# Optimization experiments

Measured on AMD Instinct MI355X. Metric: run time of the kernel, lower is better.

## Reference

```python
import jax, jax.numpy as jnp
import numpy as np

M, Q, H, L = 1, 9, 512, 2

def lstm_seq(x, w_ih, w_hh, b, reverse=False):
    # x: [B, T, Din] -> outputs [B, T, H], final (h, c) each [B, H]
    B = x.shape[0]
    h0 = jnp.zeros((B, H), x.dtype)
    xw = jnp.einsum('btd,gd->btg', x, w_ih) + b  # [B, T, 4H] input projection, precomputed
    def step(carry, xt):
        h, c = carry
        g = xt + h @ w_hh.T
        i, f, gg, o = jnp.split(g, 4, axis=-1)  # torch gate order: i, f, g, o
        c = jax.nn.sigmoid(f) * c + jax.nn.sigmoid(i) * jnp.tanh(gg)
        h = jax.nn.sigmoid(o) * jnp.tanh(c)
        return (h, c), h
    (hT, cT), hs = jax.lax.scan(step, (h0, h0), jnp.swapaxes(xw, 0, 1), reverse=reverse)
    return jnp.swapaxes(hs, 0, 1), hT, cT

def _forward(X, future_features, Y_teacher,
             enc_w_ih_l0, enc_w_hh_l0, enc_b_l0, enc_w_ih_l0r, enc_w_hh_l0r, enc_b_l0r,
             enc_w_ih_l1, enc_w_hh_l1, enc_b_l1, enc_w_ih_l1r, enc_w_hh_l1r, enc_b_l1r,
             dec_w_ih_l0, dec_w_hh_l0, dec_b_l0, dec_w_ih_l1, dec_w_hh_l1, dec_b_l1,
             bidi_w_h, bidi_b_h, out_w, out_b, horizon_span):
    B = X.shape[0]
    enc = [((enc_w_ih_l0, enc_w_hh_l0, enc_b_l0), (enc_w_ih_l0r, enc_w_hh_l0r, enc_b_l0r)),
           ((enc_w_ih_l1, enc_w_hh_l1, enc_b_l1), (enc_w_ih_l1r, enc_w_hh_l1r, enc_b_l1r))]
    inp, hs, cs = X, [], []
    for fw, bw in enc:  # bidirectional multilayer encoder
        of, hf, cf = lstm_seq(inp, *fw, reverse=False)
        ob, hb, cb = lstm_seq(inp, *bw, reverse=True)
        inp = jnp.concatenate([of, ob], axis=-1)
        hs += [hf, hb]; cs += [cf, cb]
    h = jnp.stack(hs)  # [2L, B, H], torch order (l0_fwd, l0_bwd, l1_fwd, l1_bwd)
    c = jnp.stack(cs)
    def merge(s):  # NOTE: original applies bidi_project__h / nonlin__h to BOTH h and c
        s = s.reshape(L, 2, B, H)
        s = jnp.concatenate([s[:, 0], s[:, 1]], axis=2)       # [L, B, 2H]
        s = jnp.swapaxes(s, 0, 1).reshape(B, 2 * L * H)
        s = jax.nn.elu(s @ bidi_w_h.T + bidi_b_h)             # [B, L*H]
        return jnp.swapaxes(s.reshape(B, L, H), 0, 1)         # [L, B, H]
    h, c = merge(h), merge(c)
    dec = [(dec_w_ih_l0, dec_w_hh_l0, dec_b_l0), (dec_w_ih_l1, dec_w_hh_l1, dec_b_l1)]
    def dec_step(carry, f_t):
        h, c, y_prev = carry
        x = jnp.concatenate([y_prev, f_t], axis=-1)  # [B, M + d_future_features]
        nh, nc = [], []
        for l, (w_ih, w_hh, b) in enumerate(dec):
            g = x @ w_ih.T + h[l] @ w_hh.T + b
            i, f, gg, o = jnp.split(g, 4, axis=-1)
            cl = jax.nn.sigmoid(f) * c[l] + jax.nn.sigmoid(i) * jnp.tanh(gg)
            x = jax.nn.sigmoid(o) * jnp.tanh(cl)
            nh.append(x); nc.append(cl)
        y = x @ out_w.T + out_b                       # [B, M*Q]
        return (jnp.stack(nh), jnp.stack(nc), y[:, :M]), y
    y0 = X[:, -1, :M]
    _, ys = jax.lax.scan(dec_step, (h, c, y0), jnp.swapaxes(future_features, 0, 1))
    T = future_features.shape[1]
    return jnp.swapaxes(ys, 0, 1).reshape(B, T, M, Q)

def setup_inputs() -> dict:
    key = jax.random.key(0)
    ks = iter(jax.random.split(key, 40))
    s = 0.05
    d = {
        'X': jax.random.normal(next(ks), (64, 256, 9), jnp.float32),
        'future_features': jax.random.normal(next(ks), (64, 96, 8), jnp.float32),
        'Y_teacher': jax.random.normal(next(ks), (64, 96, 1), jnp.float32),
    }
    shapes = {
        'enc_w_ih_l0': (2048, 9), 'enc_w_hh_l0': (2048, 512), 'enc_b_l0': (2048,),
        'enc_w_ih_l0r': (2048, 9), 'enc_w_hh_l0r': (2048, 512), 'enc_b_l0r': (2048,),
        'enc_w_ih_l1': (2048, 1024), 'enc_w_hh_l1': (2048, 512), 'enc_b_l1': (2048,),
        'enc_w_ih_l1r': (2048, 1024), 'enc_w_hh_l1r': (2048, 512), 'enc_b_l1r': (2048,),
        'dec_w_ih_l0': (2048, 9), 'dec_w_hh_l0': (2048, 512), 'dec_b_l0': (2048,),
        'dec_w_ih_l1': (2048, 512), 'dec_w_hh_l1': (2048, 512), 'dec_b_l1': (2048,),
        'bidi_w_h': (1024, 2048), 'bidi_b_h': (1024,),
        'out_w': (9, 512), 'out_b': (9,),
    }
    for name, shp in shapes.items():
        d[name] = jax.random.normal(next(ks), shp, jnp.float32) * s
    d['horizon_span'] = 96
    return d

def reference(X, future_features, Y_teacher,
              enc_w_ih_l0, enc_w_hh_l0, enc_b_l0, enc_w_ih_l0r, enc_w_hh_l0r, enc_b_l0r,
              enc_w_ih_l1, enc_w_hh_l1, enc_b_l1, enc_w_ih_l1r, enc_w_hh_l1r, enc_b_l1r,
              dec_w_ih_l0, dec_w_hh_l0, dec_b_l0, dec_w_ih_l1, dec_w_hh_l1, dec_b_l1,
              bidi_w_h, bidi_b_h, out_w, out_b, horizon_span):
    return _forward(X, future_features, Y_teacher,
                    enc_w_ih_l0, enc_w_hh_l0, enc_b_l0, enc_w_ih_l0r, enc_w_hh_l0r, enc_b_l0r,
                    enc_w_ih_l1, enc_w_hh_l1, enc_b_l1, enc_w_ih_l1r, enc_w_hh_l1r, enc_b_l1r,
                    dec_w_ih_l0, dec_w_hh_l0, dec_b_l0, dec_w_ih_l1, dec_w_hh_l1, dec_b_l1,
                    bidi_w_h, bidi_b_h, out_w, out_b, horizon_span)
```

## Files before the change

### kernel.cpp

```cpp
#include <hip/hip_runtime.h>


#define BLOCKS 256

typedef short bf16x8 __attribute__((ext_vector_type(8)));
typedef float f32x4  __attribute__((ext_vector_type(4)));
typedef unsigned short u16;

__device__ __forceinline__ f32x4 MFMA16(bf16x8 a, bf16x8 b, f32x4 c) {
  return __builtin_amdgcn_mfma_f32_16x16x32_bf16(a, b, c, 0, 0, 0);
}

__device__ __forceinline__ u16 bfr(float f) {
  unsigned u = __float_as_uint(f);
  u += 0x7FFFu + ((u >> 16) & 1u);
  return (u16)(u >> 16);
}
__device__ __forceinline__ bf16x8 pack8(float4 a, float4 b) {
  bf16x8 r;
  r[0] = (short)bfr(a.x); r[1] = (short)bfr(a.y); r[2] = (short)bfr(a.z); r[3] = (short)bfr(a.w);
  r[4] = (short)bfr(b.x); r[5] = (short)bfr(b.y); r[6] = (short)bfr(b.z); r[7] = (short)bfr(b.w);
  return r;
}
__device__ __forceinline__ bf16x8 loadW8(const float* p) {
  float4 a = *(const float4*)p;
  float4 b = *(const float4*)(p + 4);
  return pack8(a, b);
}
__device__ __forceinline__ float sigm(float x) { return 1.0f / (1.0f + __expf(-x)); }
__device__ __forceinline__ float tanh_f(float x) {
  float a = fabsf(x);
  float e = __expf(-2.0f * a);
  float t = (1.0f - e) / (1.0f + e);
  return x < 0.0f ? -t : t;
}
__device__ __forceinline__ float lstm_h(const float pre[4], float& c) {
  float ig = sigm(pre[0]);
  float fg = sigm(pre[1]);
  float gg = tanh_f(pre[2]);
  float og = sigm(pre[3]);
  c = fg * c + ig * gg;
  return og * tanh_f(c);
}

__device__ __forceinline__ void st_b16_coh(u16* p, u16 v) {
  unsigned uv = v;
  asm volatile("global_store_short %0, %1, off sc0 sc1" :: "v"(p), "v"(uv) : "memory");
}
__device__ __forceinline__ void st_f32_coh(float* p, float v) {
  asm volatile("global_store_dword %0, %1, off sc0 sc1" :: "v"(p), "v"(v) : "memory");
}
__device__ __forceinline__ void st_u32_coh(unsigned* p, unsigned v) {
  asm volatile("global_store_dword %0, %1, off sc0 sc1" :: "v"(p), "v"(v) : "memory");
}
__device__ __forceinline__ float ld_f32_coh(const float* p) {
  float r;
  asm volatile("global_load_dword %0, %1, off sc0 sc1\n\ts_waitcnt vmcnt(0)"
               : "=&v"(r) : "v"(p) : "memory");
  return r;
}
__device__ __forceinline__ unsigned ld_u32_coh(const unsigned* p) {
  unsigned r;
  asm volatile("global_load_dword %0, %1, off sc0 sc1\n\ts_waitcnt vmcnt(0)"
               : "=&v"(r) : "v"(p) : "memory");
  return r;
}
__device__ __forceinline__ void ld_tile_coh(const u16* base, bf16x8 f[16]) {
  asm volatile(
    "global_load_dwordx4 %0, %16, off sc0 sc1\n\t"
    "global_load_dwordx4 %1, %16, off offset:64 sc0 sc1\n\t"
    "global_load_dwordx4 %2, %16, off offset:128 sc0 sc1\n\t"
    "global_load_dwordx4 %3, %16, off offset:192 sc0 sc1\n\t"
    "global_load_dwordx4 %4, %16, off offset:256 sc0 sc1\n\t"
    "global_load_dwordx4 %5, %16, off offset:320 sc0 sc1\n\t"
    "global_load_dwordx4 %6, %16, off offset:384 sc0 sc1\n\t"
    "global_load_dwordx4 %7, %16, off offset:448 sc0 sc1\n\t"
    "global_load_dwordx4 %8, %16, off offset:512 sc0 sc1\n\t"
    "global_load_dwordx4 %9, %16, off offset:576 sc0 sc1\n\t"
    "global_load_dwordx4 %10, %16, off offset:640 sc0 sc1\n\t"
    "global_load_dwordx4 %11, %16, off offset:704 sc0 sc1\n\t"
    "global_load_dwordx4 %12, %16, off offset:768 sc0 sc1\n\t"
    "global_load_dwordx4 %13, %16, off offset:832 sc0 sc1\n\t"
    "global_load_dwordx4 %14, %16, off offset:896 sc0 sc1\n\t"
    "global_load_dwordx4 %15, %16, off offset:960 sc0 sc1\n\t"
    "s_waitcnt vmcnt(0)"
    : "=&v"(f[0]), "=&v"(f[1]), "=&v"(f[2]), "=&v"(f[3]),
      "=&v"(f[4]), "=&v"(f[5]), "=&v"(f[6]), "=&v"(f[7]),
      "=&v"(f[8]), "=&v"(f[9]), "=&v"(f[10]), "=&v"(f[11]),
      "=&v"(f[12]), "=&v"(f[13]), "=&v"(f[14]), "=&v"(f[15])
    : "v"(base)
    : "memory");
}

static constexpr size_t OFF_GO   = 32768;
static constexpr size_t OFF_YF   = 32896;
static constexpr size_t SZ_SLOT  = (size_t)64 * 512 * 2;
static constexpr size_t OFF_OF   = 65536;
static constexpr size_t OFF_OBR  = OFF_OF  + 257 * SZ_SLOT;
static constexpr size_t OFF_H1F  = OFF_OBR + 257 * SZ_SLOT;
static constexpr size_t OFF_H1B  = OFF_H1F + 2 * SZ_SLOT;
static constexpr size_t OFF_DH0  = OFF_H1B + 2 * SZ_SLOT;
static constexpr size_t OFF_DH1  = OFF_DH0 + 2 * SZ_SLOT;
static constexpr size_t OFF_SBUF = OFF_DH1 + 2 * SZ_SLOT;
static constexpr size_t OFF_CDEC = OFF_SBUF + (size_t)128 * 2048 * 4;
static constexpr size_t OFF_Y    = OFF_CDEC + (size_t)2 * 64 * 512 * 4;
static constexpr size_t WS_NEED  = OFF_Y + 256;

__device__ __forceinline__ void gridbar(char* ws, unsigned e) {
  asm volatile("s_waitcnt vmcnt(0)" ::: "memory");
  __syncthreads();
  unsigned* flags = (unsigned*)ws;
  unsigned* go    = (unsigned*)(ws + OFF_GO);
  const int tid = threadIdx.x;
  if (blockIdx.x == 0) {
    if (tid != 0) {
      const unsigned* fp = flags + (size_t)tid * 32;
      while (ld_u32_coh(fp) < e) {}
    }
    __syncthreads();
    if (tid == 0) st_u32_coh(go, e);
  } else {
    if (tid == 0) {
      st_u32_coh(flags + (size_t)blockIdx.x * 32, e);
      while (ld_u32_coh(go) < e) { __builtin_amdgcn_s_sleep(1); }
    }
    __syncthreads();
  }
}

__global__ __launch_bounds__(256, 1) void red_lstm(
    const float* __restrict__ X,   const float* __restrict__ FUT,
    const float* __restrict__ eWih0,  const float* __restrict__ eWhh0,  const float* __restrict__ eB0,
    const float* __restrict__ eWih0r, const float* __restrict__ eWhh0r, const float* __restrict__ eB0r,
    const float* __restrict__ eWih1,  const float* __restrict__ eWhh1,  const float* __restrict__ eB1,
    const float* __restrict__ eWih1r, const float* __restrict__ eWhh1r, const float* __restrict__ eB1r,
    const float* __restrict__ dWih0,  const float* __restrict__ dWhh0,  const float* __restrict__ dB0,
    const float* __restrict__ dWih1,  const float* __restrict__ dWhh1,  const float* __restrict__ dB1,
    const float* __restrict__ bW,  const float* __restrict__ bB,
    const float* __restrict__ oW,  const float* __restrict__ oB,
    float* __restrict__ OUT, char* __restrict__ ws)
{
  const int blk  = blockIdx.x;
  const int tid  = threadIdx.x;
  const int lane = tid & 63;
  const int wave = tid >> 6;
  const int n16  = lane & 15;
  const int quad = lane >> 4;
  const int rowg = wave * 16 + n16;
  const int jl   = tid & 3;
  const int bb   = tid >> 2;

  u16*   OF  = (u16*)(ws + OFF_OF);
  u16*   OBR = (u16*)(ws + OFF_OBR);
  u16*   H1F = (u16*)(ws + OFF_H1F);
  u16*   H1B = (u16*)(ws + OFF_H1B);
  u16*   DH0 = (u16*)(ws + OFF_DH0);
  u16*   DH1 = (u16*)(ws + OFF_DH1);
  float* SB  = (float*)(ws + OFF_SBUF);
  float* CD  = (float*)(ws + OFF_CDEC);
  float* YB  = (float*)(ws + OFF_Y);
  unsigned* YFLAG = (unsigned*)(ws + OFF_YF);

  __shared__ float g_s[64 * 20];
  unsigned ep = 0;

  {
    const bool fw = (blk < 128);
    const int  hb = fw ? blk : (blk - 128);
    const int  j0 = hb * 4;
    const int  col = j0 + (n16 & 3) + 512 * (n16 >> 2);
    const float* whh = fw ? eWhh0 : eWhh0r;
    const float* wih = fw ? eWih0 : eWih0r;
    const float* bia = fw ? eB0 : eB0r;
    u16* buf = fw ? OF : OBR;

    bf16x8 B[16];
    {
      const float* wr = whh + (size_t)col * 512 + quad * 8;
      #pragma unroll
      for (int kk = 0; kk < 16; ++kk) B[kk] = loadW8(wr + kk * 32);
    }
    float wr9[4][9], b4[4];
    #pragma unroll
    for (int g = 0; g < 4; ++g) {
      int cg = j0 + jl + 512 * g;
      b4[g] = bia[cg];
      #pragma unroll
      for (int k = 0; k < 9; ++k) wr9[g][k] = wih[cg * 9 + k];
    }
    float c = 0.0f;

    #pragma unroll 1
    for (int s = 0; s < 256; ++s) {
      bf16x8 T[16];
      ld_tile_coh(buf + ((size_t)s * 64 + rowg) * 512 + quad * 8, T);
      f32x4 a0 = {0.f,0.f,0.f,0.f}, a1 = {0.f,0.f,0.f,0.f};
      #pragma unroll
      for (int kk = 0; kk < 16; kk += 2) {
        a0 = MFMA16(T[kk],     B[kk],     a0);
        a1 = MFMA16(T[kk + 1], B[kk + 1], a1);
      }
      f32x4 acc = a0 + a1;
      #pragma unroll
      for (int r = 0; r < 4; ++r)
        g_s[(wave * 16 + quad * 4 + r) * 20 + n16] = acc[r];
      __syncthreads();

      const int t = fw ? s : (255 - s);
      float pre[4];
      #pragma unroll
      for (int g = 0; g < 4; ++g) pre[g] = g_s[bb * 20 + jl + 4 * g] + b4[g];
      const float* xp = X + ((size_t)bb * 256 + t) * 9;
      #pragma unroll
      for (int k = 0; k < 9; ++k) {
        float xv = xp[k];
        #pragma unroll
        for (int g = 0; g < 4; ++g) pre[g] += xv * wr9[g][k];
      }
      float h = lstm_h(pre, c);
      st_b16_coh(buf + ((size_t)(s + 1) * 64 + bb) * 512 + j0 + jl, bfr(h));
      if (s == 255) {
        int co = fw ? 0 : 512;
        st_f32_coh(SB + (size_t)bb * 2048 + co + j0 + jl, h);
        st_f32_coh(SB + (size_t)(64 + bb) * 2048 + co + j0 + jl, c);
      }
      gridbar(ws, ++ep);
    }
  }

  {
    const bool fw = (blk < 128);
    const int  hb = fw ? blk : (blk - 128);
    const int  j0 = hb * 4;
    const int  col = j0 + (n16 & 3) + 512 * (n16 >> 2);
    const float* whh = fw ? eWhh1 : eWhh1r;
    const float* wih = fw ? eWih1 : eWih1r;
    const float* bia = fw ? eB1 : eB1r;
    u16* hpp = fw ? H1F : H1B;

    bf16x8 B[48];
    {
      const float* wr = whh + (size_t)col * 512 + quad * 8;
      #pragma unroll
      for (int kk = 0; kk < 16; ++kk) B[kk] = loadW8(wr + kk * 32);
      const float* wr2 = wih + (size_t)col * 1024 + quad * 8;
      #pragma unroll
      for (int kk = 0; kk < 32; ++kk) B[16 + kk] = loadW8(wr2 + kk * 32);
    }
    float b4[4];
    #pragma unroll
    for (int g = 0; g < 4; ++g) b4[g] = bia[j0 + jl + 512 * g];
    float c = 0.0f;

    #pragma unroll 1
    for (int s = 0; s < 256; ++s) {
      const int slot_of = fw ? (s + 1)   : (256 - s);
      const int slot_ob = fw ? (256 - s) : (s + 1);
      f32x4 a0 = {0.f,0.f,0.f,0.f}, a1 = {0.f,0.f,0.f,0.f};
      {
        bf16x8 T[16];
        ld_tile_coh(hpp + ((size_t)(s & 1) * 64 + rowg) * 512 + quad * 8, T);
        #pragma unroll
        for (int kk = 0; kk < 16; kk += 2) {
          a0 = MFMA16(T[kk],     B[kk],     a0);
          a1 = MFMA16(T[kk + 1], B[kk + 1], a1);
        }
      }
      {
        bf16x8 T[16];
        ld_tile_coh(OF + ((size_t)slot_of * 64 + rowg) * 512 + quad * 8, T);
        #pragma unroll
        for (int kk = 0; kk < 16; kk += 2) {
          a0 = MFMA16(T[kk],     B[16 + kk],     a0);
          a1 = MFMA16(T[kk + 1], B[16 + kk + 1], a1);
        }
      }
      {
        bf16x8 T[16];
        ld_tile_coh(OBR + ((size_t)slot_ob * 64 + rowg) * 512 + quad * 8, T);
        #pragma unroll
        for (int kk = 0; kk < 16; kk += 2) {
          a0 = MFMA16(T[kk],     B[32 + kk],     a0);
          a1 = MFMA16(T[kk + 1], B[32 + kk + 1], a1);
        }
      }
      f32x4 acc = a0 + a1;
      #pragma unroll
      for (int r = 0; r < 4; ++r)
        g_s[(wave * 16 + quad * 4 + r) * 20 + n16] = acc[r];
      __syncthreads();

      float pre[4];
      #pragma unroll
      for (int g = 0; g < 4; ++g) pre[g] = g_s[bb * 20 + jl + 4 * g] + b4[g];
      float h = lstm_h(pre, c);
      st_b16_coh(hpp + ((size_t)((s & 1) ^ 1) * 64 + bb) * 512 + j0 + jl, bfr(h));
      if (s == 255) {
        int co = fw ? 1024 : 1536;
        st_f32_coh(SB + (size_t)bb * 2048 + co + j0 + jl, h);
        st_f32_coh(SB + (size_t)(64 + bb) * 2048 + co + j0 + jl, c);
      }
      gridbar(ws, ++ep);
    }
  }

  {
    if (blk < 128) {
      const int colm = blk * 8 + (tid & 7);
      const int rg   = tid >> 3;
      const float* wrow = bW + (size_t)colm * 2048;
      float am[4];
      #pragma unroll
      for (int r = 0; r < 4; ++r) am[r] = bB[colm];
      #pragma unroll 1
      for (int k = 0; k < 2048; k += 4) {
        float4 w = *(const float4*)(wrow + k);
        #pragma unroll
        for (int r = 0; r < 4; ++r) {
          float4 a = *(const float4*)(SB + (size_t)(rg * 4 + r) * 2048 + k);
          am[r] += a.x * w.x + a.y * w.y + a.z * w.z + a.w * w.w;
        }
      }
      const int l = colm >> 9, j = colm & 511;
      #pragma unroll
      for (int r = 0; r < 4; ++r) {
        int row = rg * 4 + r;
        float v = am[r];
        v = v > 0.f ? v : (__expf(v) - 1.0f);
        if (row < 64) {
          u16* dst = l ? DH1 : DH0;
          st_b16_coh(dst + (size_t)row * 512 + j, bfr(v));
        } else {
          st_f32_coh(CD + ((size_t)l * 64 + (row - 64)) * 512 + j, v);
        }
      }
    }
    gridbar(ws, ++ep);
  }

  {
    const bool isL0 = (blk < 128);
    const int  hb = isL0 ? blk : (blk - 128);
    const int  j0 = hb * 4;
    const int  col = j0 + (n16 & 3) + 512 * (n16 >> 2);

    bf16x8 BD[32];
    float wr9[4][9], b4[4], c;
    if (isL0) {
      const float* wr = dWhh0 + (size_t)col * 512 + quad * 8;
      #pragma unroll
      for (int kk = 0; kk < 16; ++kk) BD[kk] = loadW8(wr + kk * 32);
      #pragma unroll
      for (int g = 0; g < 4; ++g) {
        int cg = j0 + jl + 512 * g;
        b4[g] = dB0[cg];
        #pragma unroll
        for (int k = 0; k < 9; ++k) wr9[g][k] = dWih0[cg * 9 + k];
      }
      c = CD[(size_t)bb * 512 + j0 + jl];
    } else {
      const float* wr = dWhh1 + (size_t)col * 512 + quad * 8;
      #pragma unroll
      for (int kk = 0; kk < 16; ++kk) BD[kk] = loadW8(wr + kk * 32);
      const float* wr2 = dWih1 + (size_t)col * 512 + quad * 8;
      #pragma unroll
      for (int kk = 0; kk < 16; ++kk) BD[16 + kk] = loadW8(wr2 + kk * 32);
      #pragma unroll
      for (int g = 0; g < 4; ++g) b4[g] = dB1[j0 + jl + 512 * g];
      c = CD[((size_t)64 + bb) * 512 + j0 + jl];
    }
    bf16x8 OBW[16];
    float obv = 0.0f;
    if (blk == 128) {
      if (n16 < 9) {
        const float* wr = oW + (size_t)n16 * 512 + quad * 8;
        #pragma unroll
        for (int kk = 0; kk < 16; ++kk) OBW[kk] = loadW8(wr + kk * 32);
        obv = oB[n16];
      } else {
        #pragma unroll
        for (int kk = 0; kk < 16; ++kk) {
          bf16x8 z = {0,0,0,0,0,0,0,0};
          OBW[kk] = z;
        }
      }
    }

    #pragma unroll 1
    for (int t = 0; t < 96; ++t) {
      if (blk == 128 && t >= 1) {
        bf16x8 T[16];
        ld_tile_coh(DH1 + ((size_t)(t & 1) * 64 + rowg) * 512 + quad * 8, T);
        f32x4 a0 = {0.f,0.f,0.f,0.f}, a1 = {0.f,0.f,0.f,0.f};
        #pragma unroll
        for (int kk = 0; kk < 16; kk += 2) {
          a0 = MFMA16(T[kk],     OBW[kk],     a0);
          a1 = MFMA16(T[kk + 1], OBW[kk + 1], a1);
        }
        f32x4 acc = a0 + a1;
        #pragma unroll
        for (int r = 0; r < 4; ++r) {
          int b = wave * 16 + quad * 4 + r;
          float v = acc[r] + obv;
          if (n16 < 9) {
            OUT[(size_t)b * 864 + (size_t)(t - 1) * 9 + n16] = v;
            if (n16 == 0) st_f32_coh(YB + b, v);
          }
        }
        asm volatile("s_waitcnt vmcnt(0)" ::: "memory");
        __syncthreads();
        if (tid == 0) st_u32_coh(YFLAG, (unsigned)t);
      }
      if (isL0) {
        bf16x8 T[16];
        ld_tile_coh(DH0 + ((size_t)(t & 1) * 64 + rowg) * 512 + quad * 8, T);
        f32x4 a0 = {0.f,0.f,0.f,0.f}, a1 = {0.f,0.f,0.f,0.f};
        #pragma unroll
        for (int kk = 0; kk < 16; kk += 2) {
          a0 = MFMA16(T[kk],     BD[kk],     a0);
          a1 = MFMA16(T[kk + 1], BD[kk + 1], a1);
        }
        f32x4 acc = a0 + a1;
        #pragma unroll
        for (int r = 0; r < 4; ++r)
          g_s[(wave * 16 + quad * 4 + r) * 20 + n16] = acc[r];
        __syncthreads();
        if (t >= 1 && tid == 0) {
          while (ld_u32_coh(YFLAG) < (unsigned)t) {}
        }
        __syncthreads();
        float pre[4];
        #pragma unroll
        for (int g = 0; g < 4; ++g) pre[g] = g_s[bb * 20 + jl + 4 * g] + b4[g];
        float yp = (t == 0) ? X[((size_t)bb * 256 + 255) * 9] : ld_f32_coh(YB + bb);
        #pragma unroll
        for (int g = 0; g < 4; ++g) pre[g] += yp * wr9[g][0];
        const float* fp = FUT + ((size_t)bb * 96 + t) * 8;
        #pragma unroll
        for (int k = 0; k < 8; ++k) {
          float fv = fp[k];
          #pragma unroll
          for (int g = 0; g < 4; ++g) pre[g] += fv * wr9[g][k + 1];
        }
        float h = lstm_h(pre, c);
        st_b16_coh(DH0 + ((size_t)((t & 1) ^ 1) * 64 + bb) * 512 + j0 + jl, bfr(h));
      }
      gridbar(ws, ++ep);

      if (!isL0) {
        f32x4 a0 = {0.f,0.f,0.f,0.f}, a1 = {0.f,0.f,0.f,0.f};
        {
          bf16x8 T[16];
          ld_tile_coh(DH1 + ((size_t)(t & 1) * 64 + rowg) * 512 + quad * 8, T);
          #pragma unroll
          for (int kk = 0; kk < 16; kk += 2) {
            a0 = MFMA16(T[kk],     BD[kk],     a0);
            a1 = MFMA16(T[kk + 1], BD[kk + 1], a1);
          }
        }
        {
          bf16x8 T[16];
          ld_tile_coh(DH0 + ((size_t)((t & 1) ^ 1) * 64 + rowg) * 512 + quad * 8, T);
          #pragma unroll
          for (int kk = 0; kk < 16; kk += 2) {
            a0 = MFMA16(T[kk],     BD[16 + kk],     a0);
            a1 = MFMA16(T[kk + 1], BD[16 + kk + 1], a1);
          }
        }
        f32x4 acc = a0 + a1;
        #pragma unroll
        for (int r = 0; r < 4; ++r)
          g_s[(wave * 16 + quad * 4 + r) * 20 + n16] = acc[r];
        __syncthreads();
        float pre[4];
        #pragma unroll
        for (int g = 0; g < 4; ++g) pre[g] = g_s[bb * 20 + jl + 4 * g] + b4[g];
        float h = lstm_h(pre, c);
        st_b16_coh(DH1 + ((size_t)((t & 1) ^ 1) * 64 + bb) * 512 + j0 + jl, bfr(h));
      }
      gridbar(ws, ++ep);
    }

    if (blk == 128) {
      bf16x8 T[16];
      ld_tile_coh(DH1 + ((size_t)0 * 64 + rowg) * 512 + quad * 8, T);
      f32x4 a0 = {0.f,0.f,0.f,0.f}, a1 = {0.f,0.f,0.f,0.f};
      #pragma unroll
      for (int kk = 0; kk < 16; kk += 2) {
        a0 = MFMA16(T[kk],     OBW[kk],     a0);
        a1 = MFMA16(T[kk + 1], OBW[kk + 1], a1);
      }
      f32x4 acc = a0 + a1;
      #pragma unroll
      for (int r = 0; r < 4; ++r) {
        int b = wave * 16 + quad * 4 + r;
        float v = acc[r] + obv;
        if (n16 < 9) OUT[(size_t)b * 864 + (size_t)95 * 9 + n16] = v;
      }
    }
  }
}

extern "C" void kernel_launch(void* const* d_in, const int* in_sizes, int n_in,
                              void* d_out, int out_size, void* d_ws, size_t ws_size,
                              hipStream_t stream) {
  (void)in_sizes; (void)n_in; (void)out_size;
  if (ws_size < WS_NEED) return;

  const float* X      = (const float*)d_in[0];
  const float* FUT    = (const float*)d_in[1];
  const float* eWih0  = (const float*)d_in[3];
  const float* eWhh0  = (const float*)d_in[4];
  const float* eB0    = (const float*)d_in[5];
  const float* eWih0r = (const float*)d_in[6];
  const float* eWhh0r = (const float*)d_in[7];
  const float* eB0r   = (const float*)d_in[8];
  const float* eWih1  = (const float*)d_in[9];
  const float* eWhh1  = (const float*)d_in[10];
  const float* eB1    = (const float*)d_in[11];
  const float* eWih1r = (const float*)d_in[12];
  const float* eWhh1r = (const float*)d_in[13];
  const float* eB1r   = (const float*)d_in[14];
  const float* dWih0  = (const float*)d_in[15];
  const float* dWhh0  = (const float*)d_in[16];
  const float* dB0    = (const float*)d_in[17];
  const float* dWih1  = (const float*)d_in[18];
  const float* dWhh1  = (const float*)d_in[19];
  const float* dB1    = (const float*)d_in[20];
  const float* bW     = (const float*)d_in[21];
  const float* bB     = (const float*)d_in[22];
  const float* oW     = (const float*)d_in[23];
  const float* oB     = (const float*)d_in[24];

  char* ws = (char*)d_ws;
  hipMemsetAsync(ws, 0, 65536, stream);
  hipMemsetAsync(ws + OFF_OF, 0, SZ_SLOT, stream);
  hipMemsetAsync(ws + OFF_OBR, 0, SZ_SLOT, stream);
  hipMemsetAsync(ws + OFF_H1F, 0, SZ_SLOT, stream);
  hipMemsetAsync(ws + OFF_H1B, 0, SZ_SLOT, stream);

  red_lstm<<<BLOCKS, 256, 0, stream>>>(
      X, FUT,
      eWih0, eWhh0, eB0, eWih0r, eWhh0r, eB0r,
      eWih1, eWhh1, eB1, eWih1r, eWhh1r, eB1r,
      dWih0, dWhh0, dB0, dWih1, dWhh1, dB1,
      bW, bB, oW, oB,
      (float*)d_out, ws);
}
```

Before: 4.718 ms.

## Replace global grid barriers with per-step dataflow flags between LSTM groups

Swaps the centralized grid barrier for per-timestep, per-block ready flags. Each group now waits only on the specific producer steps it needs: forward/backward direction, layer 1 against layer 0, and decoder layer 0/1. All hidden-state buffers become fully versioned per step so there is no ping-pong reuse hazard. The output projection is recomputed redundantly in every decoder-L0 block to feed back y locally instead of going through a single block and a flag. The bidi merge is spread across all 256 blocks. This lets the layers pipeline and removes the barrier round-trips, at the cost of more workspace, a larger memset, and more polling traffic.

```diff
diff --git a/kernel.cpp b/kernel.cpp
--- a/kernel.cpp
+++ b/kernel.cpp
@@ -92,40 +92,52 @@
     : "memory");
 }
 
-static constexpr size_t OFF_GO   = 32768;
-static constexpr size_t OFF_YF   = 32896;
+static constexpr size_t SZ_FSTEP = 512;
+static constexpr size_t OFF_FF0  = 0;
+static constexpr size_t OFF_FB0  = OFF_FF0 + 257 * SZ_FSTEP;
+static constexpr size_t OFF_FF1  = OFF_FB0 + 257 * SZ_FSTEP;
+static constexpr size_t OFF_FB1  = OFF_FF1 + 257 * SZ_FSTEP;
+static constexpr size_t OFF_FD0  = OFF_FB1 + 257 * SZ_FSTEP;
+static constexpr size_t OFF_FD1  = OFF_FD0 + 98 * SZ_FSTEP;
+static constexpr size_t OFF_FE   = OFF_FD1 + 98 * SZ_FSTEP;
+static constexpr size_t OFF_FM   = OFF_FE + 1024;
+static constexpr size_t OFF_FEND = OFF_FM + 1024;
+
+static constexpr size_t OFF_SB   = 0xA0000;
+static constexpr size_t OFF_CD   = OFF_SB + (size_t)128 * 2048 * 4;
 static constexpr size_t SZ_SLOT  = (size_t)64 * 512 * 2;
-static constexpr size_t OFF_OF   = 65536;
+static constexpr size_t OFF_OF   = OFF_CD + (size_t)2 * 64 * 512 * 4;
 static constexpr size_t OFF_OBR  = OFF_OF  + 257 * SZ_SLOT;
 static constexpr size_t OFF_H1F  = OFF_OBR + 257 * SZ_SLOT;
-static constexpr size_t OFF_H1B  = OFF_H1F + 2 * SZ_SLOT;
-static constexpr size_t OFF_DH0  = OFF_H1B + 2 * SZ_SLOT;
-static constexpr size_t OFF_DH1  = OFF_DH0 + 2 * SZ_SLOT;
-static constexpr size_t OFF_SBUF = OFF_DH1 + 2 * SZ_SLOT;
-static constexpr size_t OFF_CDEC = OFF_SBUF + (size_t)128 * 2048 * 4;
-static constexpr size_t OFF_Y    = OFF_CDEC + (size_t)2 * 64 * 512 * 4;
-static constexpr size_t WS_NEED  = OFF_Y + 256;
-
-__device__ __forceinline__ void gridbar(char* ws, unsigned e) {
+static constexpr size_t OFF_H1B  = OFF_H1F + 257 * SZ_SLOT;
+static constexpr size_t OFF_DH0  = OFF_H1B + 257 * SZ_SLOT;
+static constexpr size_t OFF_DH1  = OFF_DH0 + 97 * SZ_SLOT;
+static constexpr size_t WS_NEED  = OFF_DH1 + 97 * SZ_SLOT;
+
+#define SLOT_U 32768
+
+__device__ __forceinline__ void poll_one(const unsigned* p) {
+  while (ld_u32_coh(p) == 0) {}
+}
+__device__ __forceinline__ void wait1(char* ws, size_t off) {
+  if (threadIdx.x < 128) poll_one((const unsigned*)(ws + off) + threadIdx.x);
+  __syncthreads();
+}
+__device__ __forceinline__ void wait2(char* ws, size_t offA, size_t offB) {
+  const unsigned* p = (threadIdx.x < 128)
+      ? (const unsigned*)(ws + offA) + threadIdx.x
+      : (const unsigned*)(ws + offB) + (threadIdx.x - 128);
+  poll_one(p);
+  __syncthreads();
+}
+__device__ __forceinline__ void wait256(char* ws, size_t off) {
+  poll_one((const unsigned*)(ws + off) + threadIdx.x);
+  __syncthreads();
+}
+__device__ __forceinline__ void publish(char* ws, size_t off, int idx) {
   asm volatile("s_waitcnt vmcnt(0)" ::: "memory");
   __syncthreads();
-  unsigned* flags = (unsigned*)ws;
-  unsigned* go    = (unsigned*)(ws + OFF_GO);
-  const int tid = threadIdx.x;
-  if (blockIdx.x == 0) {
-    if (tid != 0) {
-      const unsigned* fp = flags + (size_t)tid * 32;
-      while (ld_u32_coh(fp) < e) {}
-    }
-    __syncthreads();
-    if (tid == 0) st_u32_coh(go, e);
-  } else {
-    if (tid == 0) {
-      st_u32_coh(flags + (size_t)blockIdx.x * 32, e);
-      while (ld_u32_coh(go) < e) { __builtin_amdgcn_s_sleep(1); }
-    }
-    __syncthreads();
-  }
+  if (threadIdx.x == 0) st_u32_coh((unsigned*)(ws + off) + idx, 1u);
 }
 
 __global__ __launch_bounds__(256, 1) void red_lstm(
@@ -156,23 +168,23 @@
   u16*   H1B = (u16*)(ws + OFF_H1B);
   u16*   DH0 = (u16*)(ws + OFF_DH0);
   u16*   DH1 = (u16*)(ws + OFF_DH1);
-  float* SB  = (float*)(ws + OFF_SBUF);
-  float* CD  = (float*)(ws + OFF_CDEC);
-  float* YB  = (float*)(ws + OFF_Y);
-  unsigned* YFLAG = (unsigned*)(ws + OFF_YF);
+  float* SB  = (float*)(ws + OFF_SB);
+  float* CD  = (float*)(ws + OFF_CD);
 
   __shared__ float g_s[64 * 20];
-  unsigned ep = 0;
+  __shared__ float y_s[64];
+
+  const bool fw = (blk < 128);
+  const int  hb = fw ? blk : (blk - 128);
+  const int  j0 = hb * 4;
+  const int  col = j0 + (n16 & 3) + 512 * (n16 >> 2);
 
   {
-    const bool fw = (blk < 128);
-    const int  hb = fw ? blk : (blk - 128);
-    const int  j0 = hb * 4;
-    const int  col = j0 + (n16 & 3) + 512 * (n16 >> 2);
     const float* whh = fw ? eWhh0 : eWhh0r;
     const float* wih = fw ? eWih0 : eWih0r;
     const float* bia = fw ? eB0 : eB0r;
     u16* buf = fw ? OF : OBR;
+    const size_t fown = fw ? OFF_FF0 : OFF_FB0;
 
     bf16x8 B[16];
     {
@@ -192,8 +204,9 @@
 
     #pragma unroll 1
     for (int s = 0; s < 256; ++s) {
+      if (s > 0) wait1(ws, fown + (size_t)s * SZ_FSTEP);
       bf16x8 T[16];
-      ld_tile_coh(buf + ((size_t)s * 64 + rowg) * 512 + quad * 8, T);
+      ld_tile_coh(buf + (size_t)s * SLOT_U + rowg * 512 + quad * 8, T);
       f32x4 a0 = {0.f,0.f,0.f,0.f}, a1 = {0.f,0.f,0.f,0.f};
       #pragma unroll
       for (int kk = 0; kk < 16; kk += 2) {
@@ -218,25 +231,23 @@
         for (int g = 0; g < 4; ++g) pre[g] += xv * wr9[g][k];
       }
       float h = lstm_h(pre, c);
-      st_b16_coh(buf + ((size_t)(s + 1) * 64 + bb) * 512 + j0 + jl, bfr(h));
+      st_b16_coh(buf + (size_t)(s + 1) * SLOT_U + bb * 512 + j0 + jl, bfr(h));
       if (s == 255) {
         int co = fw ? 0 : 512;
         st_f32_coh(SB + (size_t)bb * 2048 + co + j0 + jl, h);
         st_f32_coh(SB + (size_t)(64 + bb) * 2048 + co + j0 + jl, c);
       }
-      gridbar(ws, ++ep);
+      publish(ws, fown + (size_t)(s + 1) * SZ_FSTEP, hb);
     }
   }
 
   {
-    const bool fw = (blk < 128);
-    const int  hb = fw ? blk : (blk - 128);
-    const int  j0 = hb * 4;
-    const int  col = j0 + (n16 & 3) + 512 * (n16 >> 2);
     const float* whh = fw ? eWhh1 : eWhh1r;
     const float* wih = fw ? eWih1 : eWih1r;
     const float* bia = fw ? eB1 : eB1r;
     u16* hpp = fw ? H1F : H1B;
+    const size_t fown   = fw ? OFF_FF1 : OFF_FB1;
+    const size_t fother = fw ? OFF_FB0 : OFF_FF0;
 
     bf16x8 B[48];
     {
@@ -254,12 +265,15 @@
 
     #pragma unroll 1
     for (int s = 0; s < 256; ++s) {
+      if (s == 0) wait1(ws, fother + (size_t)256 * SZ_FSTEP);
+      else        wait2(ws, fown + (size_t)s * SZ_FSTEP,
+                            fother + (size_t)(256 - s) * SZ_FSTEP);
       const int slot_of = fw ? (s + 1)   : (256 - s);
       const int slot_ob = fw ? (256 - s) : (s + 1);
       f32x4 a0 = {0.f,0.f,0.f,0.f}, a1 = {0.f,0.f,0.f,0.f};
       {
         bf16x8 T[16];
-        ld_tile_coh(hpp + ((size_t)(s & 1) * 64 + rowg) * 512 + quad * 8, T);
+        ld_tile_coh(hpp + (size_t)s * SLOT_U + rowg * 512 + quad * 8, T);
         #pragma unroll
         for (int kk = 0; kk < 16; kk += 2) {
           a0 = MFMA16(T[kk],     B[kk],     a0);
@@ -268,7 +282,7 @@
       }
       {
         bf16x8 T[16];
-        ld_tile_coh(OF + ((size_t)slot_of * 64 + rowg) * 512 + quad * 8, T);
+        ld_tile_coh(OF + (size_t)slot_of * SLOT_U + rowg * 512 + quad * 8, T);
         #pragma unroll
         for (int kk = 0; kk < 16; kk += 2) {
           a0 = MFMA16(T[kk],     B[16 + kk],     a0);
@@ -277,7 +291,7 @@
       }
       {
         bf16x8 T[16];
-        ld_tile_coh(OBR + ((size_t)slot_ob * 64 + rowg) * 512 + quad * 8, T);
+        ld_tile_coh(OBR + (size_t)slot_ob * SLOT_U + rowg * 512 + quad * 8, T);
         #pragma unroll
         for (int kk = 0; kk < 16; kk += 2) {
           a0 = MFMA16(T[kk],     B[32 + kk],     a0);
@@ -294,58 +308,53 @@
       #pragma unroll
       for (int g = 0; g < 4; ++g) pre[g] = g_s[bb * 20 + jl + 4 * g] + b4[g];
       float h = lstm_h(pre, c);
-      st_b16_coh(hpp + ((size_t)((s & 1) ^ 1) * 64 + bb) * 512 + j0 + jl, bfr(h));
+      st_b16_coh(hpp + (size_t)(s + 1) * SLOT_U + bb * 512 + j0 + jl, bfr(h));
       if (s == 255) {
         int co = fw ? 1024 : 1536;
         st_f32_coh(SB + (size_t)bb * 2048 + co + j0 + jl, h);
         st_f32_coh(SB + (size_t)(64 + bb) * 2048 + co + j0 + jl, c);
       }
-      gridbar(ws, ++ep);
+      publish(ws, fown + (size_t)(s + 1) * SZ_FSTEP, hb);
+      if (s == 255 && tid == 0)
+        st_u32_coh((unsigned*)(ws + OFF_FE) + blk, 1u);
     }
   }
 
   {
-    if (blk < 128) {
-      const int colm = blk * 8 + (tid & 7);
-      const int rg   = tid >> 3;
-      const float* wrow = bW + (size_t)colm * 2048;
-      float am[4];
-      #pragma unroll
-      for (int r = 0; r < 4; ++r) am[r] = bB[colm];
-      #pragma unroll 1
-      for (int k = 0; k < 2048; k += 4) {
-        float4 w = *(const float4*)(wrow + k);
-        #pragma unroll
-        for (int r = 0; r < 4; ++r) {
-          float4 a = *(const float4*)(SB + (size_t)(rg * 4 + r) * 2048 + k);
-          am[r] += a.x * w.x + a.y * w.y + a.z * w.z + a.w * w.w;
-        }
-      }
-      const int l = colm >> 9, j = colm & 511;
-      #pragma unroll
-      for (int r = 0; r < 4; ++r) {
-        int row = rg * 4 + r;
-        float v = am[r];
-        v = v > 0.f ? v : (__expf(v) - 1.0f);
-        if (row < 64) {
-          u16* dst = l ? DH1 : DH0;
-          st_b16_coh(dst + (size_t)row * 512 + j, bfr(v));
-        } else {
-          st_f32_coh(CD + ((size_t)l * 64 + (row - 64)) * 512 + j, v);
-        }
-      }
-    }
-    gridbar(ws, ++ep);
+    wait256(ws, OFF_FE);
+    const int colm = blk * 4 + (tid & 3);
+    const int rg   = tid >> 2;
+    const float* wrow = bW + (size_t)colm * 2048;
+    float am0 = bB[colm], am1 = am0;
+    #pragma unroll 1
+    for (int k = 0; k < 2048; k += 4) {
+      float4 w  = *(const float4*)(wrow + k);
+      float4 p0 = *(const float4*)(SB + (size_t)(rg * 2) * 2048 + k);
+      float4 p1 = *(const float4*)(SB + (size_t)(rg * 2 + 1) * 2048 + k);
+      am0 += p0.x * w.x + p0.y * w.y + p0.z * w.z + p0.w * w.w;
+      am1 += p1.x * w.x + p1.y * w.y + p1.z * w.z + p1.w * w.w;
+    }
+    const int l = colm >> 9, j = colm & 511;
+    #pragma unroll
+    for (int r = 0; r < 2; ++r) {
+      int row = rg * 2 + r;
+      float v = r ? am1 : am0;
+      v = v > 0.f ? v : (__expf(v) - 1.0f);
+      if (row < 64) {
+        u16* dst = l ? DH1 : DH0;
+        st_b16_coh(dst + (size_t)row * 512 + j, bfr(v));
+      } else {
+        st_f32_coh(CD + ((size_t)l * 64 + (row - 64)) * 512 + j, v);
+      }
+    }
+    publish(ws, OFF_FM, blk);
   }
 
   {
-    const bool isL0 = (blk < 128);
-    const int  hb = isL0 ? blk : (blk - 128);
-    const int  j0 = hb * 4;
-    const int  col = j0 + (n16 & 3) + 512 * (n16 >> 2);
-
-    bf16x8 BD[32];
-    float wr9[4][9], b4[4], c;
+    const bool isL0 = fw;
+
+    bf16x8 BD[32], OBW[16];
+    float wr9[4][9], b4[4], c, obv = 0.0f;
     if (isL0) {
       const float* wr = dWhh0 + (size_t)col * 512 + quad * 8;
       #pragma unroll
@@ -357,25 +366,10 @@
         #pragma unroll
         for (int k = 0; k < 9; ++k) wr9[g][k] = dWih0[cg * 9 + k];
       }
-      c = CD[(size_t)bb * 512 + j0 + jl];
-    } else {
-      const float* wr = dWhh1 + (size_t)col * 512 + quad * 8;
-      #pragma unroll
-      for (int kk = 0; kk < 16; ++kk) BD[kk] = loadW8(wr + kk * 32);
-      const float* wr2 = dWih1 + (size_t)col * 512 + quad * 8;
-      #pragma unroll
-      for (int kk = 0; kk < 16; ++kk) BD[16 + kk] = loadW8(wr2 + kk * 32);
-      #pragma unroll
-      for (int g = 0; g < 4; ++g) b4[g] = dB1[j0 + jl + 512 * g];
-      c = CD[((size_t)64 + bb) * 512 + j0 + jl];
-    }
-    bf16x8 OBW[16];
-    float obv = 0.0f;
-    if (blk == 128) {
       if (n16 < 9) {
-        const float* wr = oW + (size_t)n16 * 512 + quad * 8;
-        #pragma unroll
-        for (int kk = 0; kk < 16; ++kk) OBW[kk] = loadW8(wr + kk * 32);
+        const float* wo = oW + (size_t)n16 * 512 + quad * 8;
+        #pragma unroll
+        for (int kk = 0; kk < 16; ++kk) OBW[kk] = loadW8(wo + kk * 32);
         obv = oB[n16];
       } else {
         #pragma unroll
@@ -384,83 +378,113 @@
           OBW[kk] = z;
         }
       }
-    }
-
-    #pragma unroll 1
-    for (int t = 0; t < 96; ++t) {
-      if (blk == 128 && t >= 1) {
-        bf16x8 T[16];
-        ld_tile_coh(DH1 + ((size_t)(t & 1) * 64 + rowg) * 512 + quad * 8, T);
-        f32x4 a0 = {0.f,0.f,0.f,0.f}, a1 = {0.f,0.f,0.f,0.f};
-        #pragma unroll
-        for (int kk = 0; kk < 16; kk += 2) {
-          a0 = MFMA16(T[kk],     OBW[kk],     a0);
-          a1 = MFMA16(T[kk + 1], OBW[kk + 1], a1);
-        }
-        f32x4 acc = a0 + a1;
-        #pragma unroll
-        for (int r = 0; r < 4; ++r) {
-          int b = wave * 16 + quad * 4 + r;
-          float v = acc[r] + obv;
-          if (n16 < 9) {
-            OUT[(size_t)b * 864 + (size_t)(t - 1) * 9 + n16] = v;
-            if (n16 == 0) st_f32_coh(YB + b, v);
-          }
-        }
-        asm volatile("s_waitcnt vmcnt(0)" ::: "memory");
-        __syncthreads();
-        if (tid == 0) st_u32_coh(YFLAG, (unsigned)t);
-      }
-      if (isL0) {
-        bf16x8 T[16];
-        ld_tile_coh(DH0 + ((size_t)(t & 1) * 64 + rowg) * 512 + quad * 8, T);
-        f32x4 a0 = {0.f,0.f,0.f,0.f}, a1 = {0.f,0.f,0.f,0.f};
-        #pragma unroll
-        for (int kk = 0; kk < 16; kk += 2) {
-          a0 = MFMA16(T[kk],     BD[kk],     a0);
-          a1 = MFMA16(T[kk + 1], BD[kk + 1], a1);
-        }
-        f32x4 acc = a0 + a1;
-        #pragma unroll
-        for (int r = 0; r < 4; ++r)
-          g_s[(wave * 16 + quad * 4 + r) * 20 + n16] = acc[r];
-        __syncthreads();
-        if (t >= 1 && tid == 0) {
-          while (ld_u32_coh(YFLAG) < (unsigned)t) {}
-        }
-        __syncthreads();
-        float pre[4];
-        #pragma unroll
-        for (int g = 0; g < 4; ++g) pre[g] = g_s[bb * 20 + jl + 4 * g] + b4[g];
-        float yp = (t == 0) ? X[((size_t)bb * 256 + 255) * 9] : ld_f32_coh(YB + bb);
-        #pragma unroll
-        for (int g = 0; g < 4; ++g) pre[g] += yp * wr9[g][0];
-        const float* fp = FUT + ((size_t)bb * 96 + t) * 8;
-        #pragma unroll
-        for (int k = 0; k < 8; ++k) {
-          float fv = fp[k];
-          #pragma unroll
-          for (int g = 0; g < 4; ++g) pre[g] += fv * wr9[g][k + 1];
-        }
-        float h = lstm_h(pre, c);
-        st_b16_coh(DH0 + ((size_t)((t & 1) ^ 1) * 64 + bb) * 512 + j0 + jl, bfr(h));
-      }
-      gridbar(ws, ++ep);
-
-      if (!isL0) {
+    } else {
+      const float* wr = dWhh1 + (size_t)col * 512 + quad * 8;
+      #pragma unroll
+      for (int kk = 0; kk < 16; ++kk) BD[kk] = loadW8(wr + kk * 32);
+      const float* wr2 = dWih1 + (size_t)col * 512 + quad * 8;
+      #pragma unroll
+      for (int kk = 0; kk < 16; ++kk) BD[16 + kk] = loadW8(wr2 + kk * 32);
+      #pragma unroll
+      for (int g = 0; g < 4; ++g) b4[g] = dB1[j0 + jl + 512 * g];
+    }
+
+    wait256(ws, OFF_FM);
+    c = isL0 ? ld_f32_coh(CD + (size_t)bb * 512 + j0 + jl)
+             : ld_f32_coh(CD + ((size_t)64 + bb) * 512 + j0 + jl);
+
+    if (isL0) {
+      #pragma unroll 1
+      for (int t = 0; t < 96; ++t) {
+        if (t > 0) wait2(ws, OFF_FD0 + (size_t)t * SZ_FSTEP,
+                             OFF_FD1 + (size_t)t * SZ_FSTEP);
         f32x4 a0 = {0.f,0.f,0.f,0.f}, a1 = {0.f,0.f,0.f,0.f};
         {
           bf16x8 T[16];
-          ld_tile_coh(DH1 + ((size_t)(t & 1) * 64 + rowg) * 512 + quad * 8, T);
+          ld_tile_coh(DH0 + (size_t)t * SLOT_U + rowg * 512 + quad * 8, T);
           #pragma unroll
           for (int kk = 0; kk < 16; kk += 2) {
             a0 = MFMA16(T[kk],     BD[kk],     a0);
             a1 = MFMA16(T[kk + 1], BD[kk + 1], a1);
           }
         }
+        f32x4 acc = a0 + a1;
+        #pragma unroll
+        for (int r = 0; r < 4; ++r)
+          g_s[(wave * 16 + quad * 4 + r) * 20 + n16] = acc[r];
+        if (t > 0) {
+          bf16x8 T[16];
+          ld_tile_coh(DH1 + (size_t)t * SLOT_U + rowg * 512 + quad * 8, T);
+          f32x4 y0 = {0.f,0.f,0.f,0.f}, y1 = {0.f,0.f,0.f,0.f};
+          #pragma unroll
+          for (int kk = 0; kk < 16; kk += 2) {
+            y0 = MFMA16(T[kk],     OBW[kk],     y0);
+            y1 = MFMA16(T[kk + 1], OBW[kk + 1], y1);
+          }
+          f32x4 ya = y0 + y1;
+          #pragma unroll
+          for (int r = 0; r < 4; ++r) {
+            int b = wave * 16 + quad * 4 + r;
+            float v = ya[r] + obv;
+            if (n16 == 0) y_s[b] = v;
+            if (blk == 0 && n16 < 9)
+              OUT[(size_t)b * 864 + (size_t)(t - 1) * 9 + n16] = v;
+          }
+        }
+        __syncthreads();
+        float pre[4];
+        #pragma unroll
+        for (int g = 0; g < 4; ++g) pre[g] = g_s[bb * 20 + jl + 4 * g] + b4[g];
+        const float* fp = FUT + ((size_t)bb * 96 + t) * 8;
+        #pragma unroll
+        for (int k = 0; k < 8; ++k) {
+          float fv = fp[k];
+          #pragma unroll
+          for (int g = 0; g < 4; ++g) pre[g] += fv * wr9[g][k + 1];
+        }
+        float yp = (t == 0) ? X[((size_t)bb * 256 + 255) * 9] : y_s[bb];
+        #pragma unroll
+        for (int g = 0; g < 4; ++g) pre[g] += yp * wr9[g][0];
+        float h = lstm_h(pre, c);
+        st_b16_coh(DH0 + (size_t)(t + 1) * SLOT_U + bb * 512 + j0 + jl, bfr(h));
+        publish(ws, OFF_FD0 + (size_t)(t + 1) * SZ_FSTEP, hb);
+      }
+      if (blk == 0) {
+        wait1(ws, OFF_FD1 + (size_t)96 * SZ_FSTEP);
+        bf16x8 T[16];
+        ld_tile_coh(DH1 + (size_t)96 * SLOT_U + rowg * 512 + quad * 8, T);
+        f32x4 y0 = {0.f,0.f,0.f,0.f}, y1 = {0.f,0.f,0.f,0.f};
+        #pragma unroll
+        for (int kk = 0; kk < 16; kk += 2) {
+          y0 = MFMA16(T[kk],     OBW[kk],     y0);
+          y1 = MFMA16(T[kk + 1], OBW[kk + 1], y1);
+        }
+        f32x4 ya = y0 + y1;
+        #pragma unroll
+        for (int r = 0; r < 4; ++r) {
+          int b = wave * 16 + quad * 4 + r;
+          if (n16 < 9) OUT[(size_t)b * 864 + (size_t)95 * 9 + n16] = ya[r] + obv;
+        }
+      }
+    } else {
+      #pragma unroll 1
+      for (int t = 0; t < 96; ++t) {
+        if (t == 0) wait1(ws, OFF_FD0 + (size_t)1 * SZ_FSTEP);
+        else        wait2(ws, OFF_FD1 + (size_t)t * SZ_FSTEP,
+                              OFF_FD0 + (size_t)(t + 1) * SZ_FSTEP);
+        f32x4 a0 = {0.f,0.f,0.f,0.f}, a1 = {0.f,0.f,0.f,0.f};
         {
           bf16x8 T[16];
-          ld_tile_coh(DH0 + ((size_t)((t & 1) ^ 1) * 64 + rowg) * 512 + quad * 8, T);
+          ld_tile_coh(DH1 + (size_t)t * SLOT_U + rowg * 512 + quad * 8, T);
+          #pragma unroll
+          for (int kk = 0; kk < 16; kk += 2) {
+            a0 = MFMA16(T[kk],     BD[kk],     a0);
+            a1 = MFMA16(T[kk + 1], BD[kk + 1], a1);
+          }
+        }
+        {
+          bf16x8 T[16];
+          ld_tile_coh(DH0 + (size_t)(t + 1) * SLOT_U + rowg * 512 + quad * 8, T);
           #pragma unroll
           for (int kk = 0; kk < 16; kk += 2) {
             a0 = MFMA16(T[kk],     BD[16 + kk],     a0);
@@ -476,26 +500,8 @@
         #pragma unroll
         for (int g = 0; g < 4; ++g) pre[g] = g_s[bb * 20 + jl + 4 * g] + b4[g];
         float h = lstm_h(pre, c);
-        st_b16_coh(DH1 + ((size_t)((t & 1) ^ 1) * 64 + bb) * 512 + j0 + jl, bfr(h));
-      }
-      gridbar(ws, ++ep);
-    }
-
-    if (blk == 128) {
-      bf16x8 T[16];
-      ld_tile_coh(DH1 + ((size_t)0 * 64 + rowg) * 512 + quad * 8, T);
-      f32x4 a0 = {0.f,0.f,0.f,0.f}, a1 = {0.f,0.f,0.f,0.f};
-      #pragma unroll
-      for (int kk = 0; kk < 16; kk += 2) {
-        a0 = MFMA16(T[kk],     OBW[kk],     a0);
-        a1 = MFMA16(T[kk + 1], OBW[kk + 1], a1);
-      }
-      f32x4 acc = a0 + a1;
-      #pragma unroll
-      for (int r = 0; r < 4; ++r) {
-        int b = wave * 16 + quad * 4 + r;
-        float v = acc[r] + obv;
-        if (n16 < 9) OUT[(size_t)b * 864 + (size_t)95 * 9 + n16] = v;
+        st_b16_coh(DH1 + (size_t)(t + 1) * SLOT_U + bb * 512 + j0 + jl, bfr(h));
+        publish(ws, OFF_FD1 + (size_t)(t + 1) * SZ_FSTEP, hb);
       }
     }
   }
@@ -533,8 +539,8 @@
   const float* oB     = (const float*)d_in[24];
 
   char* ws = (char*)d_ws;
-  hipMemsetAsync(ws, 0, 65536, stream);
-  hipMemsetAsync(ws + OFF_OF, 0, SZ_SLOT, stream);
+  hipMemsetAsync(ws, 0, OFF_FEND, stream);
+  hipMemsetAsync(ws + OFF_OF,  0, SZ_SLOT, stream);
   hipMemsetAsync(ws + OFF_OBR, 0, SZ_SLOT, stream);
   hipMemsetAsync(ws + OFF_H1F, 0, SZ_SLOT, stream);
   hipMemsetAsync(ws + OFF_H1B, 0, SZ_SLOT, stream);
```

Measured after the change: 6.282 ms. +33.2%, slower.
